# Kernel optimization log

Measured on AMD Instinct MI355X. Metric: run time of the kernel, lower is better.

Reference implementation:

```python
import jax, jax.numpy as jnp
import numpy as np

N_NODES = 50000
N_EDGES = 800000
N_GRAPHS = 64
IN_DIM, HID1, HID2, N_CLASSES = 128, 256, 128, 10


def setup_inputs() -> dict:
    key = jax.random.key(0)
    ks = jax.random.split(key, 12)
    x = jax.random.normal(ks[0], (N_NODES, IN_DIM), dtype=jnp.float32)
    src = jax.random.randint(ks[1], (N_EDGES,), 0, N_NODES, dtype=jnp.int32)
    dst = jax.random.randint(ks[2], (N_EDGES,), 0, N_NODES, dtype=jnp.int32)
    graph_id = jnp.sort(jax.random.randint(ks[3], (N_NODES,), 0, N_GRAPHS, dtype=jnp.int32))
    s1 = 1.0 / np.sqrt(IN_DIM)
    s2 = 1.0 / np.sqrt(HID1)
    s3 = 1.0 / np.sqrt(HID2)
    s4 = 1.0 / np.sqrt(12)
    return {
        'x': x, 'src': src, 'dst': dst, 'graph_id': graph_id,
        'W1': jax.random.normal(ks[4], (IN_DIM, HID1), dtype=jnp.float32) * s1,
        'b1': jnp.zeros((HID1,), dtype=jnp.float32),
        'W2': jax.random.normal(ks[5], (HID1, HID2), dtype=jnp.float32) * s2,
        'b2': jnp.zeros((HID2,), dtype=jnp.float32),
        'Wc1': jax.random.normal(ks[6], (HID2, 12), dtype=jnp.float32) * s3,
        'bc1': jnp.zeros((12,), dtype=jnp.float32),
        'Wc2': jax.random.normal(ks[7], (12, 12), dtype=jnp.float32) * s4,
        'bc2': jnp.zeros((12,), dtype=jnp.float32),
        'Wc3': jax.random.normal(ks[8], (12, N_CLASSES), dtype=jnp.float32) * s4,
        'bc3': jnp.zeros((N_CLASSES,), dtype=jnp.float32),
    }


def _graph_conv(x, W, b, src, dst, inv_sqrt_out, inv_sqrt_in, n_nodes):
    # DGL GraphConv, norm='both': D_out^{-1/2} applied to source feats,
    # sum-aggregate over edges, then D_in^{-1/2} on destination, then +bias.
    # Weight applied first (equivalent by linearity; reduces gather traffic
    # when out_dim < in_dim, and is exactly what DGL does in that case).
    xw = (x * inv_sqrt_out[:, None]) @ W                      # [N, out]
    agg = jax.ops.segment_sum(xw[src], dst, num_segments=n_nodes)  # SpMM
    return agg * inv_sqrt_in[:, None] + b


def reference(x, src, dst, graph_id, W1, b1, W2, b2, Wc1, bc1, Wc2, bc2, Wc3, bc3):
    n = x.shape[0]
    ones_e = jnp.ones(src.shape, dtype=x.dtype)
    deg_out = jnp.maximum(jax.ops.segment_sum(ones_e, src, num_segments=n), 1.0)
    deg_in = jnp.maximum(jax.ops.segment_sum(ones_e, dst, num_segments=n), 1.0)
    inv_o = jax.lax.rsqrt(deg_out)
    inv_i = jax.lax.rsqrt(deg_in)

    h = jax.nn.relu(_graph_conv(x, W1, b1, src, dst, inv_o, inv_i, n))
    h = jax.nn.relu(_graph_conv(h, W2, b2, src, dst, inv_o, inv_i, n))

    # dgl.mean_nodes: per-graph mean over nodes of the batched graph
    gsum = jax.ops.segment_sum(h, graph_id, num_segments=N_GRAPHS)   # [G, HID2]
    cnt = jnp.maximum(jax.ops.segment_sum(jnp.ones((n,), dtype=h.dtype), graph_id, num_segments=N_GRAPHS), 1.0)
    hg = gsum / cnt[:, None]

    # tiny 3-layer MLP (no activations in between, as in the source)
    out = hg @ Wc1 + bc1
    out = out @ Wc2 + bc2
    out = out @ Wc3 + bc3
    return out
```

## Files before the change

kernel.cpp:

```cpp
#include <hip/hip_runtime.h>
#include <hip/hip_bf16.h>

#define IN_DIM 128
#define HID1 256
#define HID2 128

#define HB_BINS 12500
#define HB_WORDS 6250
#define HB_CHUNKS 64
__global__ __launch_bounds__(256) void hist_src(const int* __restrict__ src,
                                                int E, int chunk_size,
                                                int* __restrict__ part, int N) {
    __shared__ int sm[HB_WORDS];
    const int base = blockIdx.y * HB_BINS;
    const int ebeg = blockIdx.x * chunk_size;
    const int eend = min(ebeg + chunk_size, E);
    for (int w = threadIdx.x; w < HB_WORDS; w += 256) sm[w] = 0;
    __syncthreads();
    for (int e = ebeg + threadIdx.x; e < eend; e += 256) {
        int v = src[e] - base;
        if ((unsigned)v < (unsigned)HB_BINS)
            atomicAdd(&sm[v >> 1], 1 << ((v & 1) * 16));
    }
    __syncthreads();
    const int nb = min(HB_BINS, N - base);
    int* dp = part + (size_t)blockIdx.x * N + base;
    for (int w = threadIdx.x; 2 * w < nb; w += 256) {
        int packed = sm[w];
        int b = 2 * w;
        dp[b] = packed & 0xffff;
        if (b + 1 < nb) dp[b + 1] = (packed >> 16) & 0xffff;
    }
}

__global__ __launch_bounds__(256) void hist_src_reduce(const int* __restrict__ part,
                                                       int N, float* __restrict__ inv_o) {
    int b = blockIdx.x * blockDim.x + threadIdx.x;
    if (b >= N) return;
    int d = 0;
#pragma unroll 4
    for (int k = 0; k < HB_CHUNKS; ++k) d += part[(size_t)k * N + b];
    inv_o[b] = rsqrtf((float)max(d, 1));
}

#define BK_SHIFT 8
#define NBUCK 196
#define NCHUNK 256
#define PADCAP 2048
__global__ __launch_bounds__(256) void coarse_hist(const int* __restrict__ dst, int E,
                                                   int chunk_size, int* __restrict__ ccnt,
                                                   float* __restrict__ hg, int hg_n) {
    __shared__ int cnt[NBUCK];
    if (blockIdx.x == 0)
        for (int i = threadIdx.x; i < hg_n; i += 256) hg[i] = 0.f;
    for (int i = threadIdx.x; i < NBUCK; i += 256) cnt[i] = 0;
    __syncthreads();
    int ebeg = blockIdx.x * chunk_size, eend = min(ebeg + chunk_size, E);
    for (int e = ebeg + threadIdx.x; e < eend; e += 256)
        atomicAdd(&cnt[dst[e] >> BK_SHIFT], 1);
    __syncthreads();
    for (int i = threadIdx.x; i < NBUCK; i += 256) ccnt[blockIdx.x * NBUCK + i] = cnt[i];
}

__global__ __launch_bounds__(NCHUNK) void coarse_col(const int* __restrict__ ccnt,
                                                     int* __restrict__ coffpre,
                                                     int* __restrict__ ctot) {
    __shared__ int sm[NCHUNK];
    const int b = blockIdx.x, t = threadIdx.x;
    int v = ccnt[t * NBUCK + b];
    sm[t] = v;
    __syncthreads();
#pragma unroll
    for (int off = 1; off < NCHUNK; off <<= 1) {
        int u = (t >= off) ? sm[t - off] : 0;
        __syncthreads();
        sm[t] += u;
        __syncthreads();
    }
    coffpre[t * NBUCK + b] = sm[t] - v;
    if (t == NCHUNK - 1) ctot[b] = sm[t];
}

__device__ __forceinline__ void scan_bbase(const int* __restrict__ ctot, int* sm, int* bbase) {
    const int t = threadIdx.x;
    int v = (t < NBUCK) ? ctot[t] : 0;
    sm[t] = v;
    __syncthreads();
#pragma unroll
    for (int off = 1; off < 256; off <<= 1) {
        int u = (t >= off) ? sm[t - off] : 0;
        __syncthreads();
        sm[t] += u;
        __syncthreads();
    }
    if (t < NBUCK) bbase[t] = sm[t] - v;
    __syncthreads();
}

__global__ __launch_bounds__(256) void scat_a(const int* __restrict__ src,
                                              const int* __restrict__ dst, int E,
                                              int chunk_size,
                                              const int* __restrict__ coffpre,
                                              const int* __restrict__ ctot,
                                              int2* __restrict__ pairs) {
    __shared__ int sm[256];
    __shared__ int bbase[NBUCK];
    __shared__ int lcur[NBUCK];
    scan_bbase(ctot, sm, bbase);
    for (int i = threadIdx.x; i < NBUCK; i += 256)
        lcur[i] = bbase[i] + coffpre[blockIdx.x * NBUCK + i];
    __syncthreads();
    int ebeg = blockIdx.x * chunk_size, eend = min(ebeg + chunk_size, E);
    for (int e = ebeg + threadIdx.x; e < eend; e += 256) {
        int d = dst[e];
        int p = atomicAdd(&lcur[d >> BK_SHIFT], 1);
        pairs[p] = make_int2(src[e], d);
    }
}

__global__ __launch_bounds__(256) void scat_b(const int2* __restrict__ pairs,
                                              const int* __restrict__ ctot, int N,
                                              int* __restrict__ rowb,
                                              int* __restrict__ rowe,
                                              float* __restrict__ inv_i,
                                              int* __restrict__ csr_src) {
    __shared__ int sm[256];
    __shared__ int bbase[NBUCK];
    __shared__ int cnt[1 << BK_SHIFT];
    __shared__ int cur[1 << BK_SHIFT];
    const int b = blockIdx.x, t = threadIdx.x;
    scan_bbase(ctot, sm, bbase);
    const int segBase = bbase[b];
    const int segEnd = segBase + ctot[b];
    const int pSegBase = ((bbase[b] + 7) & ~7) + b * PADCAP;
    const int nb0 = b << BK_SHIFT;
    const int nbn = min(256, N - nb0);
    cnt[t] = 0;
    __syncthreads();
    for (int j = segBase + t; j < segEnd; j += 256)
        atomicAdd(&cnt[pairs[j].y - nb0], 1);
    __syncthreads();
    int v = cnt[t];
    int pv = (v + 7) & ~7;
    sm[t] = pv;
    __syncthreads();
#pragma unroll
    for (int off = 1; off < 256; off <<= 1) {
        int u = (t >= off) ? sm[t - off] : 0;
        __syncthreads();
        sm[t] += u;
        __syncthreads();
    }
    int pexcl = sm[t] - pv;
    int pbeg = pSegBase + pexcl;
    cur[t] = pbeg;
    if (t < nbn) {
        rowb[nb0 + t] = pbeg;
        rowe[nb0 + t] = pbeg + pv;
        inv_i[nb0 + t] = rsqrtf((float)max(v, 1));
        for (int k = v; k < pv; ++k) csr_src[pbeg + k] = N;
    }
    __syncthreads();
    for (int j = segBase + t; j < segEnd; j += 256) {
        int2 pr = pairs[j];
        int p = atomicAdd(&cur[pr.y - nb0], 1);
        csr_src[p] = pr.x;
    }
}

__global__ void cvt_all(const float* __restrict__ x, const float* __restrict__ inv_o,
                        __hip_bfloat16* __restrict__ x_bf, int n4x,
                        __hip_bfloat16* __restrict__ xw2_bf, int N,
                        const float* __restrict__ W1, __hip_bfloat16* __restrict__ W1t,
                        const float* __restrict__ W2, __hip_bfloat16* __restrict__ W2t) {
    const int S1 = IN_DIM * HID1;
    const int S2 = HID1 * HID2;
    int i = blockIdx.x * blockDim.x + threadIdx.x;
    if (i < n4x) {
        float s = inv_o[i >> 5];
        float4 v = reinterpret_cast<const float4*>(x)[i];
        __hip_bfloat16 b0 = __float2bfloat16(v.x * s);
        __hip_bfloat16 b1 = __float2bfloat16(v.y * s);
        __hip_bfloat16 b2 = __float2bfloat16(v.z * s);
        __hip_bfloat16 b3 = __float2bfloat16(v.w * s);
        ushort4 o = make_ushort4(*(unsigned short*)&b0, *(unsigned short*)&b1,
                                 *(unsigned short*)&b2, *(unsigned short*)&b3);
        reinterpret_cast<ushort4*>(x_bf)[i] = o;
    } else if (i < n4x + 32) {
        reinterpret_cast<ushort4*>(x_bf)[(size_t)N * 32 + (i - n4x)] = make_ushort4(0, 0, 0, 0);
    } else if (i < n4x + 64) {
        reinterpret_cast<ushort4*>(xw2_bf)[(size_t)N * 32 + (i - n4x - 32)] = make_ushort4(0, 0, 0, 0);
    } else {
        int idx = i - n4x - 64;
        if (idx < S1) {
            int k = idx / HID1, n = idx - k * HID1;
            W1t[n * IN_DIM + k] = __float2bfloat16(W1[idx]);
        } else if (idx < S1 + S2) {
            int j = idx - S1;
            int k = j / HID2, n = j - k * HID2;
            W2t[n * HID1 + k] = __float2bfloat16(W2[j]);
        }
    }
}

__device__ __forceinline__ void bf2_unpack(unsigned int p, float& lo, float& hi) {
    lo = __uint_as_float(p << 16);
    hi = __uint_as_float(p & 0xffff0000u);
}

__device__ __forceinline__ void gather_row(const unsigned int* __restrict__ fp,
                                           const int* __restrict__ csr_src,
                                           int beg, int end, int lane,
                                           float& A0, float& A1) {
    float a0 = 0.f, a1 = 0.f;
    int j = beg;
    for (; j + 16 <= end; j += 16) {
        int4 i0 = *reinterpret_cast<const int4*>(csr_src + j);
        int4 i1 = *reinterpret_cast<const int4*>(csr_src + j + 4);
        int4 i2 = *reinterpret_cast<const int4*>(csr_src + j + 8);
        int4 i3 = *reinterpret_cast<const int4*>(csr_src + j + 12);
        unsigned int p0  = fp[(size_t)i0.x * 64 + lane];
        unsigned int p1  = fp[(size_t)i0.y * 64 + lane];
        unsigned int p2  = fp[(size_t)i0.z * 64 + lane];
        unsigned int p3  = fp[(size_t)i0.w * 64 + lane];
        unsigned int p4  = fp[(size_t)i1.x * 64 + lane];
        unsigned int p5  = fp[(size_t)i1.y * 64 + lane];
        unsigned int p6  = fp[(size_t)i1.z * 64 + lane];
        unsigned int p7  = fp[(size_t)i1.w * 64 + lane];
        unsigned int p8  = fp[(size_t)i2.x * 64 + lane];
        unsigned int p9  = fp[(size_t)i2.y * 64 + lane];
        unsigned int p10 = fp[(size_t)i2.z * 64 + lane];
        unsigned int p11 = fp[(size_t)i2.w * 64 + lane];
        unsigned int p12 = fp[(size_t)i3.x * 64 + lane];
        unsigned int p13 = fp[(size_t)i3.y * 64 + lane];
        unsigned int p14 = fp[(size_t)i3.z * 64 + lane];
        unsigned int p15 = fp[(size_t)i3.w * 64 + lane];
        float lo, hi;
        bf2_unpack(p0,  lo, hi); a0 += lo; a1 += hi;
        bf2_unpack(p1,  lo, hi); a0 += lo; a1 += hi;
        bf2_unpack(p2,  lo, hi); a0 += lo; a1 += hi;
        bf2_unpack(p3,  lo, hi); a0 += lo; a1 += hi;
        bf2_unpack(p4,  lo, hi); a0 += lo; a1 += hi;
        bf2_unpack(p5,  lo, hi); a0 += lo; a1 += hi;
        bf2_unpack(p6,  lo, hi); a0 += lo; a1 += hi;
        bf2_unpack(p7,  lo, hi); a0 += lo; a1 += hi;
        bf2_unpack(p8,  lo, hi); a0 += lo; a1 += hi;
        bf2_unpack(p9,  lo, hi); a0 += lo; a1 += hi;
        bf2_unpack(p10, lo, hi); a0 += lo; a1 += hi;
        bf2_unpack(p11, lo, hi); a0 += lo; a1 += hi;
        bf2_unpack(p12, lo, hi); a0 += lo; a1 += hi;
        bf2_unpack(p13, lo, hi); a0 += lo; a1 += hi;
        bf2_unpack(p14, lo, hi); a0 += lo; a1 += hi;
        bf2_unpack(p15, lo, hi); a0 += lo; a1 += hi;
    }
    if (j + 8 <= end) {
        int4 i0 = *reinterpret_cast<const int4*>(csr_src + j);
        int4 i1 = *reinterpret_cast<const int4*>(csr_src + j + 4);
        unsigned int p0 = fp[(size_t)i0.x * 64 + lane];
        unsigned int p1 = fp[(size_t)i0.y * 64 + lane];
        unsigned int p2 = fp[(size_t)i0.z * 64 + lane];
        unsigned int p3 = fp[(size_t)i0.w * 64 + lane];
        unsigned int p4 = fp[(size_t)i1.x * 64 + lane];
        unsigned int p5 = fp[(size_t)i1.y * 64 + lane];
        unsigned int p6 = fp[(size_t)i1.z * 64 + lane];
        unsigned int p7 = fp[(size_t)i1.w * 64 + lane];
        float lo, hi;
        bf2_unpack(p0, lo, hi); a0 += lo; a1 += hi;
        bf2_unpack(p1, lo, hi); a0 += lo; a1 += hi;
        bf2_unpack(p2, lo, hi); a0 += lo; a1 += hi;
        bf2_unpack(p3, lo, hi); a0 += lo; a1 += hi;
        bf2_unpack(p4, lo, hi); a0 += lo; a1 += hi;
        bf2_unpack(p5, lo, hi); a0 += lo; a1 += hi;
        bf2_unpack(p6, lo, hi); a0 += lo; a1 += hi;
        bf2_unpack(p7, lo, hi); a0 += lo; a1 += hi;
        j += 8;
    }
    for (; j < end; ++j) {
        unsigned int p0 = fp[(size_t)csr_src[j] * 64 + lane];
        float lo, hi;
        bf2_unpack(p0, lo, hi); a0 += lo; a1 += hi;
    }
    A0 = a0; A1 = a1;
}

__global__ __launch_bounds__(256) void spmm_kernel(const __hip_bfloat16* __restrict__ feat,
                                                   const int* __restrict__ rowb,
                                                   const int* __restrict__ rowe,
                                                   const int* __restrict__ csr_src,
                                                   __hip_bfloat16* __restrict__ out_bf, int N) {
    const int node = blockIdx.x * 4 + (threadIdx.x >> 6);
    if (node >= N) return;
    const int lane = threadIdx.x & 63;
    const unsigned int* fp = (const unsigned int*)feat;
    float a0, a1;
    gather_row(fp, csr_src, rowb[node], rowe[node], lane, a0, a1);
    __hip_bfloat16 b0 = __float2bfloat16(a0);
    __hip_bfloat16 b1 = __float2bfloat16(a1);
    unsigned int packed = (unsigned int)(*(unsigned short*)&b0) |
                          ((unsigned int)(*(unsigned short*)&b1) << 16);
    ((unsigned int*)out_bf)[(size_t)node * 64 + lane] = packed;
}

#define SP_NODES 4
__global__ __launch_bounds__(256) void spmm_pool_kernel(const __hip_bfloat16* __restrict__ feat,
                                                        const int* __restrict__ rowb,
                                                        const int* __restrict__ rowe,
                                                        const int* __restrict__ csr_src,
                                                        const float* __restrict__ inv_i,
                                                        const float* __restrict__ b2,
                                                        const int* __restrict__ graph_id,
                                                        int N, float* __restrict__ hg_sum) {
    const int wave = blockIdx.x * 4 + (threadIdx.x >> 6);
    const int lane = threadIdx.x & 63;
    const int n0 = wave * SP_NODES;
    if (n0 >= N) return;
    const int n1 = min(n0 + SP_NODES, N);
    const unsigned int* fp = (const unsigned int*)feat;
    const float bias0 = b2[2 * lane];
    const float bias1 = b2[2 * lane + 1];
    int g = graph_id[n0];
    float p0s = 0.f, p1s = 0.f;
    for (int node = n0; node < n1; ++node) {
        int gi = graph_id[node];
        if (gi != g) {
            atomicAdd(&hg_sum[g * HID2 + 2 * lane], p0s);
            atomicAdd(&hg_sum[g * HID2 + 2 * lane + 1], p1s);
            p0s = p1s = 0.f;
            g = gi;
        }
        float a0, a1;
        gather_row(fp, csr_src, rowb[node], rowe[node], lane, a0, a1);
        float ii = inv_i[node];
        p0s += fmaxf(a0 * ii + bias0, 0.f);
        p1s += fmaxf(a1 * ii + bias1, 0.f);
    }
    atomicAdd(&hg_sum[g * HID2 + 2 * lane], p0s);
    atomicAdd(&hg_sum[g * HID2 + 2 * lane + 1], p1s);
}

#define GBM 128
#define GBN 128
#define GBK 32
#define LPAD 40
typedef __attribute__((ext_vector_type(4))) float floatx4;
typedef __attribute__((ext_vector_type(8))) short shortx8;

__global__ __launch_bounds__(256) void mfma_gemm_kernel(const __hip_bfloat16* __restrict__ A,
                                                        const __hip_bfloat16* __restrict__ Bt,
                                                        __hip_bfloat16* __restrict__ C,
                                                        const float* __restrict__ scaleR,
                                                        const float* __restrict__ bias,
                                                        const float* __restrict__ scaleO,
                                                        int M, int Nn, int K, int doRelu) {
    __shared__ __align__(16) __hip_bfloat16 As[GBM * LPAD];
    __shared__ __align__(16) __hip_bfloat16 Bs[GBN * LPAD];
    const int tid = threadIdx.x;
    const int bm = blockIdx.x * GBM;
    const int bn = blockIdx.y * GBN;
    const int wid = tid >> 6;
    const int lane = tid & 63;
    const int wm = (wid & 1) * 64;
    const int wn = (wid >> 1) * 64;
    const int lrow = lane & 15;
    const int quad = lane >> 4;

    floatx4 acc[4][4] = {};

    for (int k0 = 0; k0 < K; k0 += GBK) {
#pragma unroll
        for (int it = 0; it < 2; ++it) {
            int slot = tid + (it << 8);
            int r = slot >> 2;
            int cc = (slot & 3) << 3;
            int gr = bm + r;
            float4 v = make_float4(0.f, 0.f, 0.f, 0.f);
            if (gr < M) v = *reinterpret_cast<const float4*>(A + (size_t)gr * K + k0 + cc);
            *reinterpret_cast<float4*>(&As[r * LPAD + cc]) = v;
        }
#pragma unroll
        for (int it = 0; it < 2; ++it) {
            int slot = tid + (it << 8);
            int r = slot >> 2;
            int cc = (slot & 3) << 3;
            float4 v = *reinterpret_cast<const float4*>(Bt + (size_t)(bn + r) * K + k0 + cc);
            *reinterpret_cast<float4*>(&Bs[r * LPAD + cc]) = v;
        }
        __syncthreads();

        shortx8 af[4], bf[4];
#pragma unroll
        for (int i = 0; i < 4; ++i)
            af[i] = *reinterpret_cast<const shortx8*>(&As[(wm + i * 16 + lrow) * LPAD + quad * 8]);
#pragma unroll
        for (int i = 0; i < 4; ++i)
            bf[i] = *reinterpret_cast<const shortx8*>(&Bs[(wn + i * 16 + lrow) * LPAD + quad * 8]);
#pragma unroll
        for (int im = 0; im < 4; ++im)
#pragma unroll
            for (int in = 0; in < 4; ++in)
                acc[im][in] = __builtin_amdgcn_mfma_f32_16x16x32_bf16(af[im], bf[in], acc[im][in], 0, 0, 0);
        __syncthreads();
    }

    float bv[4];
#pragma unroll
    for (int in = 0; in < 4; ++in)
        bv[in] = bias ? bias[bn + wn + in * 16 + lrow] : 0.f;

#pragma unroll
    for (int im = 0; im < 4; ++im) {
#pragma unroll
        for (int reg = 0; reg < 4; ++reg) {
            int r = bm + wm + im * 16 + quad * 4 + reg;
            if (r >= M) continue;
            float sR = scaleR ? scaleR[r] : 1.f;
            float sO = scaleO ? scaleO[r] : 1.f;
#pragma unroll
            for (int in = 0; in < 4; ++in) {
                int cc = bn + wn + in * 16 + lrow;
                float v = acc[im][in][reg] * sR + bv[in];
                if (doRelu) v = fmaxf(v, 0.f);
                v *= sO;
                C[(size_t)r * Nn + cc] = __float2bfloat16(v);
            }
        }
    }
}

__device__ __forceinline__ int lower_bound_i(const int* a, int n, int key) {
    int lo = 0, hi = n;
    while (lo < hi) {
        int mid = (lo + hi) >> 1;
        if (a[mid] < key) lo = mid + 1; else hi = mid;
    }
    return lo;
}

__global__ __launch_bounds__(64) void mlp_kernel(const float* __restrict__ hg_sum,
                                                 const int* __restrict__ graph_id, int n,
                                                 const float* __restrict__ Wc1, const float* __restrict__ bc1,
                                                 const float* __restrict__ Wc2, const float* __restrict__ bc2,
                                                 const float* __restrict__ Wc3, const float* __restrict__ bc3,
                                                 float* __restrict__ out) {
    const int g = blockIdx.x;
    const int t = threadIdx.x;
    __shared__ float h[HID2];
    __shared__ float t1[12];
    __shared__ float t2[12];
    __shared__ float s_inv_cnt;
    if (t == 0) {
        int beg = lower_bound_i(graph_id, n, g);
        int end = lower_bound_i(graph_id, n, g + 1);
        int c = end - beg;
        s_inv_cnt = 1.0f / (float)max(c, 1);
    }
    __syncthreads();
    const float ic = s_inv_cnt;
    for (int i = t; i < HID2; i += 64) h[i] = hg_sum[g * HID2 + i] * ic;
    __syncthreads();
    if (t < 12) {
        float a = bc1[t];
        for (int k = 0; k < HID2; ++k) a += h[k] * Wc1[k * 12 + t];
        t1[t] = a;
    }
    __syncthreads();
    if (t < 12) {
        float a = bc2[t];
        for (int k = 0; k < 12; ++k) a += t1[k] * Wc2[k * 12 + t];
        t2[t] = a;
    }
    __syncthreads();
    if (t < 10) {
        float a = bc3[t];
        for (int k = 0; k < 12; ++k) a += t2[k] * Wc3[k * 10 + t];
        out[g * 10 + t] = a;
    }
}

extern "C" void kernel_launch(void* const* d_in, const int* in_sizes, int n_in,
                              void* d_out, int out_size, void* d_ws, size_t ws_size,
                              hipStream_t stream) {
    const float* x        = (const float*)d_in[0];
    const int*   src      = (const int*)d_in[1];
    const int*   dst      = (const int*)d_in[2];
    const int*   graph_id = (const int*)d_in[3];
    const float* W1       = (const float*)d_in[4];
    const float* b1       = (const float*)d_in[5];
    const float* W2       = (const float*)d_in[6];
    const float* b2       = (const float*)d_in[7];
    const float* Wc1      = (const float*)d_in[8];
    const float* bc1      = (const float*)d_in[9];
    const float* Wc2      = (const float*)d_in[10];
    const float* bc2      = (const float*)d_in[11];
    const float* Wc3      = (const float*)d_in[12];
    const float* bc3      = (const float*)d_in[13];
    float* out = (float*)d_out;

    const int N = in_sizes[0] / IN_DIM;
    const int E = in_sizes[1];
    const int G = out_size / 10;

    char* ws = (char*)d_ws;
    size_t off = 0;
    auto alloc = [&](size_t bytes) -> char* {
        char* p = ws + off;
        off = (off + bytes + 255) & ~(size_t)255;
        return p;
    };
    float* inv_i   = (float*)alloc((size_t)N * 4);
    float* inv_o   = (float*)alloc((size_t)N * 4);
    int*   rowb    = (int*)alloc((size_t)N * 4);
    int*   rowe    = (int*)alloc((size_t)N * 4);
    int*   ccnt    = (int*)alloc((size_t)NCHUNK * NBUCK * 4);
    int*   coffpre = (int*)alloc((size_t)NCHUNK * NBUCK * 4);
    int*   ctot    = (int*)alloc((size_t)NBUCK * 4);
    int2*  pairs   = (int2*)alloc((size_t)E * 8);
    int*   csr_src = (int*)alloc(((size_t)E + (size_t)NBUCK * PADCAP + 64) * 4);
    float* hg      = (float*)alloc((size_t)G * HID2 * 4);
    __hip_bfloat16* x_bf    = (__hip_bfloat16*)alloc((size_t)(N + 1) * IN_DIM * 2);
    __hip_bfloat16* W1t     = (__hip_bfloat16*)alloc((size_t)IN_DIM * HID1 * 2);
    __hip_bfloat16* W2t     = (__hip_bfloat16*)alloc((size_t)HID1 * HID2 * 2);
    __hip_bfloat16* agg1_bf = (__hip_bfloat16*)alloc((size_t)N * IN_DIM * 2);
    __hip_bfloat16* h1_bf   = (__hip_bfloat16*)alloc((size_t)N * HID1 * 2);
    __hip_bfloat16* xw2_bf  = (__hip_bfloat16*)alloc((size_t)(N + 1) * HID2 * 2);

    int* part = (int*)h1_bf;

    const int hchunk = (E + HB_CHUNKS - 1) / HB_CHUNKS;
    const int n_ranges = (N + HB_BINS - 1) / HB_BINS;
    hist_src<<<dim3(HB_CHUNKS, n_ranges), 256, 0, stream>>>(src, E, hchunk, part, N);
    hist_src_reduce<<<(N + 255) / 256, 256, 0, stream>>>(part, N, inv_o);

    const int schunk = (E + NCHUNK - 1) / NCHUNK;
    coarse_hist<<<NCHUNK, 256, 0, stream>>>(dst, E, schunk, ccnt, hg, G * HID2);
    coarse_col<<<NBUCK, NCHUNK, 0, stream>>>(ccnt, coffpre, ctot);
    scat_a<<<NCHUNK, 256, 0, stream>>>(src, dst, E, schunk, coffpre, ctot, pairs);
    scat_b<<<NBUCK, 256, 0, stream>>>(pairs, ctot, N, rowb, rowe, inv_i, csr_src);

    const int n4x = N * IN_DIM / 4;
    cvt_all<<<(n4x + 64 + IN_DIM * HID1 + HID1 * HID2 + 255) / 256, 256, 0, stream>>>(
        x, inv_o, x_bf, n4x, xw2_bf, N, W1, W1t, W2, W2t);

    spmm_kernel<<<(N + 3) / 4, 256, 0, stream>>>(x_bf, rowb, rowe, csr_src, agg1_bf, N);
    mfma_gemm_kernel<<<dim3((N + GBM - 1) / GBM, HID1 / GBN), 256, 0, stream>>>(
        agg1_bf, W1t, h1_bf, inv_i, b1, inv_o, N, HID1, IN_DIM, 1);

    mfma_gemm_kernel<<<dim3((N + GBM - 1) / GBM, HID2 / GBN), 256, 0, stream>>>(
        h1_bf, W2t, xw2_bf, nullptr, nullptr, nullptr, N, HID2, HID1, 0);
    const int npw = (N + SP_NODES - 1) / SP_NODES;
    spmm_pool_kernel<<<(npw + 3) / 4, 256, 0, stream>>>(xw2_bf, rowb, rowe, csr_src, inv_i, b2,
                                                        graph_id, N, hg);

    mlp_kernel<<<G, 64, 0, stream>>>(hg, graph_id, N, Wc1, bc1, Wc2, bc2, Wc3, bc3, out);
}
```

Measured before the change: 277.4 us.

## Fuse degree reduction into conversion, use direct global-to-LDS loads in GEMM

The separate hist_src_reduce kernel is removed. Its per-node reduction of partial source-degree counts now runs inside cvt_all, where each block reduces 8 nodes through shared memory before scaling and converting x to bf16. The MFMA GEMM loads its tiles with global_load_lds, which writes straight into LDS without a register round-trip, and drops the LDS padding, which may cause bank conflicts on the fragment reads. The M-bounds check on A loads is also removed, so the last partial tile reads past row N. The pooling SpMM now handles 8 nodes per wave instead of 4, which cuts atomic traffic but leaves fewer waves.

```diff
diff --git a/kernel.cpp b/kernel.cpp
--- a/kernel.cpp
+++ b/kernel.cpp
@@ -31,16 +31,6 @@
         dp[b] = packed & 0xffff;
         if (b + 1 < nb) dp[b + 1] = (packed >> 16) & 0xffff;
     }
-}
-
-__global__ __launch_bounds__(256) void hist_src_reduce(const int* __restrict__ part,
-                                                       int N, float* __restrict__ inv_o) {
-    int b = blockIdx.x * blockDim.x + threadIdx.x;
-    if (b >= N) return;
-    int d = 0;
-#pragma unroll 4
-    for (int k = 0; k < HB_CHUNKS; ++k) d += part[(size_t)k * N + b];
-    inv_o[b] = rsqrtf((float)max(d, 1));
 }
 
 #define BK_SHIFT 8
@@ -168,16 +158,35 @@
     }
 }
 
-__global__ void cvt_all(const float* __restrict__ x, const float* __restrict__ inv_o,
+__global__ void cvt_all(const float* __restrict__ x, const int* __restrict__ part,
+                        float* __restrict__ inv_o,
                         __hip_bfloat16* __restrict__ x_bf, int n4x,
                         __hip_bfloat16* __restrict__ xw2_bf, int N,
                         const float* __restrict__ W1, __hip_bfloat16* __restrict__ W1t,
                         const float* __restrict__ W2, __hip_bfloat16* __restrict__ W2t) {
     const int S1 = IN_DIM * HID1;
     const int S2 = HID1 * HID2;
-    int i = blockIdx.x * blockDim.x + threadIdx.x;
-    if (i < n4x) {
-        float s = inv_o[i >> 5];
+    const int t = threadIdx.x;
+    int i = blockIdx.x * 256 + t;
+    if ((int)(blockIdx.x * 256) < n4x) {
+        __shared__ int sm[256];
+        __shared__ float ls[8];
+        const int r0 = blockIdx.x * 8;
+        const int rl = t >> 5;
+        const int ch = t & 31;
+        const int node = r0 + rl;
+        sm[t] = part[(size_t)ch * N + node] + part[(size_t)(ch + 32) * N + node];
+        __syncthreads();
+        if (t < 8) {
+            int d = 0;
+#pragma unroll
+            for (int k = 0; k < 32; ++k) d += sm[t * 32 + k];
+            float iv = rsqrtf((float)max(d, 1));
+            inv_o[r0 + t] = iv;
+            ls[t] = iv;
+        }
+        __syncthreads();
+        float s = ls[t >> 5];
         float4 v = reinterpret_cast<const float4*>(x)[i];
         __hip_bfloat16 b0 = __float2bfloat16(v.x * s);
         __hip_bfloat16 b1 = __float2bfloat16(v.y * s);
@@ -301,7 +310,7 @@
     ((unsigned int*)out_bf)[(size_t)node * 64 + lane] = packed;
 }
 
-#define SP_NODES 4
+#define SP_NODES 8
 __global__ __launch_bounds__(256) void spmm_pool_kernel(const __hip_bfloat16* __restrict__ feat,
                                                         const int* __restrict__ rowb,
                                                         const int* __restrict__ rowe,
@@ -341,9 +350,14 @@
 #define GBM 128
 #define GBN 128
 #define GBK 32
-#define LPAD 40
 typedef __attribute__((ext_vector_type(4))) float floatx4;
 typedef __attribute__((ext_vector_type(8))) short shortx8;
+
+__device__ __forceinline__ void gload_lds16(const void* g, void* l) {
+    __builtin_amdgcn_global_load_lds(
+        (const __attribute__((address_space(1))) unsigned int*)g,
+        (__attribute__((address_space(3))) unsigned int*)l, 16, 0, 0);
+}
 
 __global__ __launch_bounds__(256) void mfma_gemm_kernel(const __hip_bfloat16* __restrict__ A,
                                                         const __hip_bfloat16* __restrict__ Bt,
@@ -352,8 +366,8 @@
                                                         const float* __restrict__ bias,
                                                         const float* __restrict__ scaleO,
                                                         int M, int Nn, int K, int doRelu) {
-    __shared__ __align__(16) __hip_bfloat16 As[GBM * LPAD];
-    __shared__ __align__(16) __hip_bfloat16 Bs[GBN * LPAD];
+    __shared__ __align__(16) __hip_bfloat16 As[GBM * GBK];
+    __shared__ __align__(16) __hip_bfloat16 Bs[GBN * GBK];
     const int tid = threadIdx.x;
     const int bm = blockIdx.x * GBM;
     const int bn = blockIdx.y * GBN;
@@ -368,32 +382,30 @@
 
     for (int k0 = 0; k0 < K; k0 += GBK) {
 #pragma unroll
-        for (int it = 0; it < 2; ++it) {
-            int slot = tid + (it << 8);
+        for (int c = 0; c < 2; ++c) {
+            int slot = c * 256 + tid;
             int r = slot >> 2;
-            int cc = (slot & 3) << 3;
-            int gr = bm + r;
-            float4 v = make_float4(0.f, 0.f, 0.f, 0.f);
-            if (gr < M) v = *reinterpret_cast<const float4*>(A + (size_t)gr * K + k0 + cc);
-            *reinterpret_cast<float4*>(&As[r * LPAD + cc]) = v;
+            int ko = (slot & 3) << 3;
+            gload_lds16(A + (size_t)(bm + r) * K + k0 + ko,
+                        (char*)As + c * 4096 + wid * 1024);
         }
 #pragma unroll
-        for (int it = 0; it < 2; ++it) {
-            int slot = tid + (it << 8);
+        for (int c = 0; c < 2; ++c) {
+            int slot = c * 256 + tid;
             int r = slot >> 2;
-            int cc = (slot & 3) << 3;
-            float4 v = *reinterpret_cast<const float4*>(Bt + (size_t)(bn + r) * K + k0 + cc);
-            *reinterpret_cast<float4*>(&Bs[r * LPAD + cc]) = v;
+            int ko = (slot & 3) << 3;
+            gload_lds16(Bt + (size_t)(bn + r) * K + k0 + ko,
+                        (char*)Bs + c * 4096 + wid * 1024);
         }
         __syncthreads();
 
         shortx8 af[4], bf[4];
 #pragma unroll
         for (int i = 0; i < 4; ++i)
-            af[i] = *reinterpret_cast<const shortx8*>(&As[(wm + i * 16 + lrow) * LPAD + quad * 8]);
+            af[i] = *reinterpret_cast<const shortx8*>(&As[(wm + i * 16 + lrow) * GBK + quad * 8]);
 #pragma unroll
         for (int i = 0; i < 4; ++i)
-            bf[i] = *reinterpret_cast<const shortx8*>(&Bs[(wn + i * 16 + lrow) * LPAD + quad * 8]);
+            bf[i] = *reinterpret_cast<const shortx8*>(&Bs[(wn + i * 16 + lrow) * GBK + quad * 8]);
 #pragma unroll
         for (int im = 0; im < 4; ++im)
 #pragma unroll
@@ -529,7 +541,6 @@
     const int hchunk = (E + HB_CHUNKS - 1) / HB_CHUNKS;
     const int n_ranges = (N + HB_BINS - 1) / HB_BINS;
     hist_src<<<dim3(HB_CHUNKS, n_ranges), 256, 0, stream>>>(src, E, hchunk, part, N);
-    hist_src_reduce<<<(N + 255) / 256, 256, 0, stream>>>(part, N, inv_o);
 
     const int schunk = (E + NCHUNK - 1) / NCHUNK;
     coarse_hist<<<NCHUNK, 256, 0, stream>>>(dst, E, schunk, ccnt, hg, G * HID2);
@@ -539,7 +550,7 @@
 
     const int n4x = N * IN_DIM / 4;
     cvt_all<<<(n4x + 64 + IN_DIM * HID1 + HID1 * HID2 + 255) / 256, 256, 0, stream>>>(
-        x, inv_o, x_bf, n4x, xw2_bf, N, W1, W1t, W2, W2t);
+        x, part, inv_o, x_bf, n4x, xw2_bf, N, W1, W1t, W2, W2t);
 
     spmm_kernel<<<(N + 3) / 4, 256, 0, stream>>>(x_bf, rowb, rowe, csr_src, agg1_bf, N);
     mfma_gemm_kernel<<<dim3((N + GBM - 1) / GBM, HID1 / GBN), 256, 0, stream>>>(
```

Result: faster. 260.0 us (-6.3%).
